# Optimization experiments

Measured on AMD Instinct MI355X. Metric: run time of the kernel, lower is better.

## Reference

```python
import jax, jax.numpy as jnp
import numpy as np
import math

T, B = 512, 32
QD, SD, H, NH = 128, 256, 512, 8
NQ, NS, NSUB = 30000, 400, 8
DKEY = QD + 2 * SD      # 640
DVAL = 4 * SD + QD      # 1152
P = H + 2 * SD + QD     # 1152 (pred_in_feature)
DH = H // NH            # 64
NEG = -1e32


def _layernorm(x, g, b, eps=1e-5):
    mu = jnp.mean(x, axis=-1, keepdims=True)
    var = jnp.mean((x - mu) ** 2, axis=-1, keepdims=True)
    return (x - mu) * jax.lax.rsqrt(var + eps) * g + b


def setup_inputs() -> dict:
    key = jax.random.key(0)
    ks = iter(jax.random.split(key, 48))
    def nrm(shape, scale=0.05):
        return (scale * jax.random.normal(next(ks), shape)).astype(jnp.float32)
    inp = {}
    inp['ans'] = jax.random.randint(next(ks), (T, B), 1, 5, dtype=jnp.int32)
    inp['correct_ans'] = jax.random.randint(next(ks), (T, B), 1, 5, dtype=jnp.int32)
    inp['labels'] = jax.random.randint(next(ks), (T, B), 0, 2, dtype=jnp.int32)
    inp['mask'] = jnp.ones((T, B), jnp.float32)
    inp['q_ids'] = jax.random.randint(next(ks), (T, B), 0, NQ, dtype=jnp.int32)
    inp['subject_ids'] = jax.random.randint(next(ks), (T, B, NSUB), 0, NS, dtype=jnp.int32)
    inp['subject_mask'] = (jax.random.uniform(next(ks), (T, B, NSUB)) < 0.7).astype(jnp.float32)
    inp['Eq'] = nrm((NQ, QD)); inp['Es'] = nrm((NS, SD))
    inp['Ea'] = nrm((4, SD)); inp['El'] = nrm((2, SD))
    inp['Wq'] = nrm((H, DKEY)); inp['bq'] = jnp.zeros((H,), jnp.float32)
    inp['Wk'] = nrm((H, DKEY)); inp['bk'] = jnp.zeros((H,), jnp.float32)
    inp['Wv'] = nrm((H, DVAL)); inp['bv'] = jnp.zeros((H,), jnp.float32)
    inp['Wo'] = nrm((H, H)); inp['bo'] = jnp.zeros((H,), jnp.float32)
    inp['ln1_g'] = jnp.ones((H,), jnp.float32); inp['ln1_b'] = jnp.zeros((H,), jnp.float32)
    inp['W1'] = nrm((H, H)); inp['b1'] = jnp.zeros((H,), jnp.float32)
    inp['W2'] = nrm((H, H)); inp['b2'] = jnp.zeros((H,), jnp.float32)
    inp['ln2_g'] = jnp.ones((H,), jnp.float32); inp['ln2_b'] = jnp.zeros((H,), jnp.float32)
    inp['gammas'] = jnp.zeros((NH, 1, 1), jnp.float32)
    inp['L1W'] = nrm((P, P)); inp['L1b'] = jnp.zeros((P,), jnp.float32)
    inp['L2W'] = nrm((P, P)); inp['L2b'] = jnp.zeros((P,), jnp.float32)
    inp['OW'] = nrm((1, P)); inp['Ob'] = jnp.zeros((1,), jnp.float32)
    return inp


def _forward(ans, correct_ans, labels, q_ids, subject_ids,
             mask, subject_mask, Eq, Es, Ea, El,
             Wq, bq, Wk, bk, Wv, bv, Wo, bo, ln1_g, ln1_b,
             W1, b1, W2, b2, ln2_g, ln2_b, gammas,
             L1W, L1b, L2W, L2b, OW, Ob):
    m3 = mask[:, :, None]                                   # [T,B,1]
    subjects = jnp.sum(Es[subject_ids] * subject_mask[..., None], axis=2)   # [T,B,SD]
    questions = Eq[q_ids]                                   # [T,B,QD]
    ans_embed = Ea[ans - 1] * m3
    ca_embed = Ea[correct_ans - 1]
    lab_embed = El[labels] * m3
    query = jnp.concatenate([questions, subjects, ca_embed], axis=-1)       # [T,B,DKEY]
    value = jnp.concatenate([lab_embed, ans_embed, ca_embed, questions, subjects], axis=-1)  # [T,B,DVAL]
    # note: original applies q_linear to kk and k_linear to qq (qq==kk==query here); akt=True => no pos-embed
    q = (query @ Wq.T + bq).reshape(T, B, NH, DH).transpose(1, 2, 0, 3)     # [B,NH,T,DH]
    k = (query @ Wk.T + bk).reshape(T, B, NH, DH).transpose(1, 2, 0, 3)
    v = (value @ Wv.T + bv).reshape(T, B, NH, DH).transpose(1, 2, 0, 3)
    scores = jnp.einsum('bhqd,bhkd->bhqk', q, k) / math.sqrt(DH)            # [B,NH,T,T]
    scores = jnp.where(mask.T[:, None, None, :] == 0, NEG, scores)
    # exponential distance decay (Softplus-gamma), applied AFTER the key-pad fill as in the original
    idx = jnp.arange(T)
    pe = jnp.sqrt(jnp.abs(idx[None, :] - idx[:, None]).astype(jnp.float32)) # [T,T]
    total_effect = jnp.clip(jnp.exp(pe[None] * (-jax.nn.softplus(gammas))), 1e-5, 1e5)  # [NH,T,T]
    scores = scores * total_effect[None]
    causal_bad = jnp.triu(jnp.ones((T, T), bool))            # upper incl. diagonal is masked
    scores = jnp.where(causal_bad, NEG, scores)
    scores = jax.nn.softmax(scores, axis=-1)
    scores = scores.at[:, :, 0, :].set(0.0)                  # pad-zero first query row
    attn = jnp.einsum('bhqk,bhkd->bhqd', scores, v)
    concat = attn.transpose(2, 0, 1, 3).reshape(T, B, H)
    out = _layernorm(concat @ Wo.T + bo, ln1_g, ln1_b)
    ffn = jax.nn.relu(out @ W1.T + b1) @ W2.T + b2
    out = out + _layernorm(ffn, ln2_g, ln2_b)
    pred = jnp.concatenate([out, questions, subjects, ca_embed], axis=-1)   # [T,B,P]
    h = jax.nn.relu(pred @ L1W.T + L1b)
    h = jax.nn.relu(h @ L2W.T + L2b)
    logits = ((h + pred) @ OW.T + Ob)[..., 0]                # [T,B]
    y = labels.astype(jnp.float32)
    bce = jnp.maximum(logits, 0.0) - logits * y + jnp.log1p(jnp.exp(-jnp.abs(logits)))
    loss = jnp.mean(bce * mask) / jnp.mean(mask)
    return loss


def reference(ans, correct_ans, labels, mask, q_ids, subject_ids, subject_mask,
              Eq, Es, Ea, El, Wq, bq, Wk, bk, Wv, bv, Wo, bo, ln1_g, ln1_b,
              W1, b1, W2, b2, ln2_g, ln2_b, gammas, L1W, L1b, L2W, L2b, OW, Ob):
    return _forward(ans, correct_ans, labels, q_ids, subject_ids,
                    mask, subject_mask, Eq, Es, Ea, El,
                    Wq, bq, Wk, bk, Wv, bv, Wo, bo, ln1_g, ln1_b,
                    W1, b1, W2, b2, ln2_g, ln2_b, gammas,
                    L1W, L1b, L2W, L2b, OW, Ob)
```

## Files before the change

kernel.cpp:

```cpp
#include <hip/hip_runtime.h>
#include <math.h>

#define T_LEN 512
#define B_SZ  32
#define NHEAD 8
#define DHEAD 64
#define H_DIM 512
#define TBTOK 16384
#define P_DIM 1152
#define P_PAD 1280

typedef unsigned short ushort_t;
typedef short short8 __attribute__((ext_vector_type(8)));
typedef float f32x4 __attribute__((ext_vector_type(4)));

__device__ __forceinline__ ushort_t f2bf(float f) {
    union { float f; unsigned int u; } v; v.f = f;
    unsigned int r = v.u + 0x7fffu + ((v.u >> 16) & 1u);
    return (ushort_t)(r >> 16);
}
__device__ __forceinline__ float bf2f(ushort_t h) {
    union { unsigned int u; float f; } v; v.u = ((unsigned int)h) << 16;
    return v.f;
}
__device__ __forceinline__ void gload_lds16(const void* g, void* l) {
    __builtin_amdgcn_global_load_lds(
        (const __attribute__((address_space(1))) void*)g,
        (__attribute__((address_space(3))) void*)l, 16, 0, 0);
}

__global__ __launch_bounds__(256) void convert_weights(
    const float* __restrict__ wq, const float* __restrict__ wk,
    const float* __restrict__ wv, const float* __restrict__ wo,
    const float* __restrict__ w1, const float* __restrict__ w2,
    ushort_t* __restrict__ dst, float* __restrict__ accum)
{
    if (blockIdx.x == 0 && threadIdx.x < 2) accum[threadIdx.x] = 0.f;
    const unsigned int offs[7] = {0u, 327680u, 655360u, 1245184u, 1507328u,
                                  1769472u, 2031616u};
    unsigned int c = (blockIdx.x * 256 + threadIdx.x) * 4;
    const float* srcs[6] = {wq, wk, wv, wo, w1, w2};
    int s = 0;
#pragma unroll
    for (int i = 0; i < 5; i++) s += (c >= offs[i + 1]) ? 1 : 0;
    float4 v = *(const float4*)(srcs[s] + (c - offs[s]));
    ushort4 o;
    o.x = f2bf(v.x); o.y = f2bf(v.y); o.z = f2bf(v.z); o.w = f2bf(v.w);
    *(ushort4*)(dst + c) = o;
}

__global__ __launch_bounds__(256) void pad_weights(
    const float* __restrict__ l1, const float* __restrict__ l2,
    const float* __restrict__ L1b, const float* __restrict__ L2b,
    const float* __restrict__ OW,
    ushort_t* __restrict__ l1d, ushort_t* __restrict__ l2d,
    float* __restrict__ L1bp, float* __restrict__ L2bp, float* __restrict__ OWp)
{
    int blk = blockIdx.x;
    if (blk < 1440) {
        int o4 = (blk * 256 + threadIdx.x) * 4;
        int row = o4 / 1152;
        int col = o4 - row * 1152;
        ushort4 o; o.x = 0; o.y = 0; o.z = 0; o.w = 0;
        if (row < 1152) {
            float4 v = *(const float4*)(l1 + (size_t)row * 1152 + col);
            o.x = f2bf(v.x); o.y = f2bf(v.y); o.z = f2bf(v.z); o.w = f2bf(v.w);
        }
        *(ushort4*)(l1d + o4) = o;
    } else if (blk < 3040) {
        int o4 = ((blk - 1440) * 256 + threadIdx.x) * 4;
        int row = o4 / 1280;
        int col = o4 - row * 1280;
        ushort4 o; o.x = 0; o.y = 0; o.z = 0; o.w = 0;
        if (row < 1152 && col < 1152) {
            float4 v = *(const float4*)(l2 + (size_t)row * 1152 + col);
            o.x = f2bf(v.x); o.y = f2bf(v.y); o.z = f2bf(v.z); o.w = f2bf(v.w);
        }
        *(ushort4*)(l2d + o4) = o;
    } else {
        for (int i = threadIdx.x; i < P_PAD; i += 256) {
            L1bp[i] = (i < P_DIM) ? L1b[i] : 0.f;
            L2bp[i] = (i < P_DIM) ? L2b[i] : 0.f;
            OWp[i]  = (i < P_DIM) ? OW[i]  : 0.f;
        }
    }
}

__global__ __launch_bounds__(256) void embed_kernel(
    const int* __restrict__ ans, const int* __restrict__ cans,
    const int* __restrict__ labels, const float* __restrict__ mask,
    const int* __restrict__ qids, const int* __restrict__ sids,
    const float* __restrict__ smask,
    const float* __restrict__ Eq, const float* __restrict__ Es,
    const float* __restrict__ Ea, const float* __restrict__ El,
    ushort_t* __restrict__ pred_bf, ushort_t* __restrict__ value_bf,
    const float* __restrict__ OW, const float* __restrict__ Ob,
    float* __restrict__ lgits)
{
    __shared__ float red[4];
    int m = blockIdx.x;
    int tid = threadIdx.x;
    float mval = mask[m];
    int qid = qids[m];
    int a   = ans[m] - 1;
    int ca  = cans[m] - 1;
    int lb  = labels[m];
    ushort_t* pr = pred_bf  + (size_t)m * P_DIM;
    ushort_t* vr = value_bf + (size_t)m * P_DIM;

    float part = 0.f;
    if (tid < 128) {
        ushort_t qv = f2bf(Eq[(size_t)qid * 128 + tid]);
        pr[512 + tid] = qv;
        vr[768 + tid] = qv;
        part = bf2f(qv) * OW[512 + tid];
    }
    int d = tid;
    float s = 0.f;
#pragma unroll
    for (int j = 0; j < 8; j++) {
        int  sid = sids[m * 8 + j];
        float sm = smask[m * 8 + j];
        s += Es[(size_t)sid * 256 + d] * sm;
    }
    ushort_t sb = f2bf(s);
    pr[640 + d] = sb;
    vr[896 + d] = sb;
    ushort_t cab = f2bf(Ea[ca * 256 + d]);
    pr[896 + d] = cab;
    vr[512 + d] = cab;
    vr[256 + d] = f2bf(Ea[a * 256 + d] * mval);
    vr[0   + d] = f2bf(El[lb * 256 + d] * mval);

    part = fmaf(bf2f(sb),  OW[640 + d], part);
    part = fmaf(bf2f(cab), OW[896 + d], part);
#pragma unroll
    for (int off = 32; off >= 1; off >>= 1) part += __shfl_xor(part, off, 64);
    if ((tid & 63) == 0) red[tid >> 6] = part;
    __syncthreads();
    if (tid == 0) lgits[m] = red[0] + red[1] + red[2] + red[3] + Ob[0];
}

template<int JC, int MODE, bool RELU>
__global__ __launch_bounds__(512, 2) void gemm4p(
    const ushort_t* __restrict__ A, int lda,
    const ushort_t* __restrict__ W, int ldw,
    const float* __restrict__ bias, const float* __restrict__ bias2,
    ushort_t* __restrict__ Cb, ushort_t* __restrict__ Cb2, int ldc, int K,
    const float* __restrict__ OW, float* __restrict__ lg)
{
    constexpr int BN = JC * 64;
    __shared__ __align__(16) ushort_t As2[2][2][256 * 32];
    __shared__ __align__(16) ushort_t Bs2[2][2][BN * 32];

    const int m0 = blockIdx.x * 256;
    const int n0 = blockIdx.y * BN;
    const int tid  = threadIdx.x;
    const int wave = tid >> 6;
    const int lane = tid & 63;
    const int wm = wave >> 2, wn = wave & 3;
    const int fr   = lane & 15;
    const int quad = lane >> 4;
    const int csw  = ((quad + ((fr >> 1) & 3)) & 3) * 8;

    const int slr = lane >> 2;
    const int sc  = (((lane & 3) - ((lane >> 3) & 3)) & 3) * 8;
    const ushort_t* Asrc;
    size_t aRS;
    if (MODE == 4) {
        Asrc = A + ((size_t)(((m0 & 511) + slr) << 5) + (m0 >> 9)) * lda + sc;
        aRS  = (size_t)32 * lda;
    } else {
        Asrc = A + (size_t)(m0 + slr) * lda + sc;
        aRS  = (size_t)lda;
    }
    const ushort_t* Wsrc = W + (size_t)(n0 + slr) * ldw + sc;
    const int NT = K >> 6;

    auto stA = [&](int t, int kh) {
#pragma unroll
        for (int n = 0; n < 2; n++) {
            int rl = (wave + 8 * n) << 4;
            gload_lds16(Asrc + (size_t)rl * aRS + (t * 64 + kh * 32),
                        &As2[t & 1][kh][rl * 32]);
        }
    };
    auto stB = [&](int t, int kh) {
#pragma unroll
        for (int n = 0; n < JC / 2; n++) {
            int rl = (wave + 8 * n) << 4;
            gload_lds16(Wsrc + (size_t)rl * ldw + (t * 64 + kh * 32),
                        &Bs2[t & 1][kh][rl * 32]);
        }
        if (JC & 1) {
            if (wave < 4) {
                int rl = (wave + 8 * (JC / 2)) << 4;
                gload_lds16(Wsrc + (size_t)rl * ldw + (t * 64 + kh * 32),
                            &Bs2[t & 1][kh][rl * 32]);
            }
        }
    };
    auto waitSteady = [&]() {
        if (JC == 2)      asm volatile("s_waitcnt vmcnt(3)" ::: "memory");
        else if (JC == 4) asm volatile("s_waitcnt vmcnt(4)" ::: "memory");
        else {
            if (wave < 4) asm volatile("s_waitcnt vmcnt(5)" ::: "memory");
            else          asm volatile("s_waitcnt vmcnt(4)" ::: "memory");
        }
    };

    f32x4 acc[8][JC] = {};

    stA(0, 0); stB(0, 0); stA(0, 1); stB(0, 1);
    if (NT > 1) { stA(1, 0); stB(1, 0); }
    if (NT > 2) waitSteady();
    else        asm volatile("s_waitcnt vmcnt(0)" ::: "memory");
    __builtin_amdgcn_s_barrier();

    short8 af[4], ag[4], bf[JC];
    for (int t = 0; t < NT; ++t) {
        const int db = t & 1;
        const ushort_t* Ar0 = &As2[db][0][0];
        const ushort_t* Ar1 = &As2[db][1][0];
        const ushort_t* Br0 = &Bs2[db][0][0];
        const ushort_t* Br1 = &Bs2[db][1][0];

#pragma unroll
        for (int i = 0; i < 4; i++)
            af[i] = *(const short8*)&Ar0[(wm * 128 + i * 16 + fr) * 32 + csw];
#pragma unroll
        for (int j = 0; j < JC; j++)
            bf[j] = *(const short8*)&Br0[(wn * (JC * 16) + j * 16 + fr) * 32 + csw];
        if (t + 1 < NT) stA(t + 1, 1);
#pragma unroll
        for (int i = 0; i < 4; i++)
#pragma unroll
            for (int j = 0; j < JC; j++)
                acc[i][j] = __builtin_amdgcn_mfma_f32_16x16x32_bf16(
                    af[i], bf[j], acc[i][j], 0, 0, 0);
#pragma unroll
        for (int i = 0; i < 4; i++)
            ag[i] = *(const short8*)&Ar0[(wm * 128 + 64 + i * 16 + fr) * 32 + csw];
        if (t + 1 < NT) stB(t + 1, 1);
#pragma unroll
        for (int i = 0; i < 4; i++)
#pragma unroll
            for (int j = 0; j < JC; j++)
                acc[4 + i][j] = __builtin_amdgcn_mfma_f32_16x16x32_bf16(
                    ag[i], bf[j], acc[4 + i][j], 0, 0, 0);
        __builtin_amdgcn_s_barrier();

#pragma unroll
        for (int i = 0; i < 4; i++)
            af[i] = *(const short8*)&Ar1[(wm * 128 + i * 16 + fr) * 32 + csw];
#pragma unroll
        for (int j = 0; j < JC; j++)
            bf[j] = *(const short8*)&Br1[(wn * (JC * 16) + j * 16 + fr) * 32 + csw];
        if (t + 2 < NT) stA(t + 2, 0);
#pragma unroll
        for (int i = 0; i < 4; i++)
#pragma unroll
            for (int j = 0; j < JC; j++)
                acc[i][j] = __builtin_amdgcn_mfma_f32_16x16x32_bf16(
                    af[i], bf[j], acc[i][j], 0, 0, 0);
#pragma unroll
        for (int i = 0; i < 4; i++)
            ag[i] = *(const short8*)&Ar1[(wm * 128 + 64 + i * 16 + fr) * 32 + csw];
        if (t + 2 < NT) stB(t + 2, 0);
#pragma unroll
        for (int i = 0; i < 4; i++)
#pragma unroll
            for (int j = 0; j < JC; j++)
                acc[4 + i][j] = __builtin_amdgcn_mfma_f32_16x16x32_bf16(
                    ag[i], bf[j], acc[4 + i][j], 0, 0, 0);
        if (t + 2 < NT) waitSteady();
        else            asm volatile("s_waitcnt vmcnt(0)" ::: "memory");
        __builtin_amdgcn_s_barrier();
    }

    const int nbase = n0 + wn * (JC * 16);

    if (MODE == 3) {
#pragma unroll
        for (int ii = 0; ii < 8; ii++)
#pragma unroll
            for (int r = 0; r < 4; r++) {
                int row = m0 + wm * 128 + (ii >> 2) * 64 + (ii & 3) * 16 + quad * 4 + r;
                float part = 0.f;
#pragma unroll
                for (int j = 0; j < JC; j++) {
                    int col = nbase + j * 16 + fr;
                    float v = fmaxf(acc[ii][j][r] + bias[col], 0.f);
                    part = fmaf(v, OW[col], part);
                }
                part += __shfl_xor(part, 1, 64);
                part += __shfl_xor(part, 2, 64);
                part += __shfl_xor(part, 4, 64);
                part += __shfl_xor(part, 8, 64);
                if (fr == 0) atomicAdd(&lg[row], part);
            }
        return;
    }

    if (MODE == 5) {
        bool side = (nbase >= 512);
        const float* bp = side ? bias2 : bias;
        const int boff  = nbase & 511;
        const float scl = side ? 1.f : 0.125f;
        ushort_t* base  = side ? Cb2 : Cb;
        const int h = (nbase >> 6) & 7;
        ushort_t* etw = ((ushort_t*)As2) + wave * (16 * 72);
#pragma unroll
        for (int ii = 0; ii < 8; ii++) {
#pragma unroll
            for (int r = 0; r < 4; r++)
#pragma unroll
                for (int j = 0; j < 4; j++) {
                    float v = (acc[ii][j][r] + bp[boff + j * 16 + fr]) * scl;
                    etw[(quad * 4 + r) * 72 + j * 16 + fr] = f2bf(v);
                }
            int rowb = m0 + wm * 128 + (ii >> 2) * 64 + (ii & 3) * 16;
#pragma unroll
            for (int u = lane; u < 128; u += 64) {
                int rr = u >> 3, cc = (u & 7) * 8;
                int row = rowb + rr;
                int tq = row >> 5, b = row & 31;
                short8 val = *(const short8*)&etw[rr * 72 + cc];
                *(short8*)&base[(((size_t)(b * 8 + h)) << 15) + ((size_t)tq << 6) + cc] = val;
            }
        }
        return;
    }

    if (MODE == 4) {
        ushort_t* etw = ((ushort_t*)As2) + wave * (32 * 72);
        const int h = nbase >> 6;
        const int dbase = nbase & 63;
#pragma unroll
        for (int mh = 0; mh < 2; mh++) {
#pragma unroll
            for (int i = 0; i < 4; i++)
#pragma unroll
                for (int r = 0; r < 4; r++) {
                    int rl = i * 16 + quad * 4 + r;
#pragma unroll
                    for (int j = 0; j < 2; j++) {
                        int cl = j * 16 + fr;
                        float v = acc[mh * 4 + i][j][r] + bias[nbase + cl];
                        etw[cl * 72 + rl] = f2bf(v);
                    }
                }
            int mbase = m0 + wm * 128 + mh * 64;
            int b = mbase >> 9, t0 = mbase & 511;
            size_t obase = (((size_t)(b * 8 + h)) << 15) + ((size_t)dbase << 9) + t0;
#pragma unroll
            for (int u = lane; u < 256; u += 64) {
                int dr = u >> 3, cc = (u & 7) * 8;
                short8 val = *(const short8*)&etw[dr * 72 + cc];
                *(short8*)&Cb[obase + ((size_t)dr << 9) + cc] = val;
            }
        }
        return;
    }

    {
        constexpr int STR = JC * 16 + 8;
        constexpr int CPR = 2 * JC;
        ushort_t* etw = ((ushort_t*)As2) + wave * (16 * STR);
#pragma unroll
        for (int ii = 0; ii < 8; ii++) {
#pragma unroll
            for (int r = 0; r < 4; r++)
#pragma unroll
                for (int j = 0; j < JC; j++) {
                    float v = acc[ii][j][r] + bias[nbase + j * 16 + fr];
                    if (RELU) v = fmaxf(v, 0.f);
                    etw[(quad * 4 + r) * STR + j * 16 + fr] = f2bf(v);
                }
            int rowb = m0 + wm * 128 + (ii >> 2) * 64 + (ii & 3) * 16;
#pragma unroll
            for (int u = lane; u < 16 * CPR; u += 64) {
                int rr = u / CPR;
                int cc = u - rr * CPR;
                short8 val = *(const short8*)&etw[rr * STR + cc * 8];
                *(short8*)&Cb[(size_t)(rowb + rr) * ldc + nbase + cc * 8] = val;
            }
        }
    }
}

__global__ __launch_bounds__(256) void attn_mfma(
    const ushort_t* __restrict__ qb, const ushort_t* __restrict__ kb,
    const ushort_t* __restrict__ vtb, const float* __restrict__ mask,
    const float* __restrict__ gammas, ushort_t* __restrict__ attnc)
{
    __shared__ __align__(16) ushort_t kbuf[2][64 * 64];
    __shared__ __align__(16) ushort_t vbuf[2][64 * 64];
    __shared__ __align__(16) ushort_t ps[4][16][72];
    __shared__ float decayF[512];
    __shared__ float mneg[512];

    const int bh  = blockIdx.x;
    const int b   = bh >> 3;
    const int h   = bh & 7;
    const int qt0 = (7 - blockIdx.y) * 64;
    const int tid  = threadIdx.x;
    const int wave = tid >> 6;
    const int lane = tid & 63;
    const int fr   = lane & 15;
    const int quad = lane >> 4;

    {
        float g  = gammas[h];
        float sp = (g > 20.f) ? g : log1pf(expf(g));
        for (int i = tid; i < 512; i += 256) {
            decayF[i] = fmaxf(exp2f(-sp * 1.44269504f * sqrtf((float)i)), 1e-5f)
                        * 1.44269504f;
            mneg[i]   = (mask[(size_t)i * B_SZ + b] == 0.f) ? -1e32f : 0.f;
        }
    }

    const int qr0 = qt0 + wave * 16;
    const ushort_t* qbase = qb  + ((size_t)bh << 15);
    const ushort_t* kbase = kb  + ((size_t)bh << 15);
    const ushort_t* vbase = vtb + ((size_t)bh << 15);

    short8 af0 = *(const short8*)(qbase + (size_t)(qr0 + fr) * 64 + quad * 8);
    short8 af1 = *(const short8*)(qbase + (size_t)(qr0 + fr) * 64 + 32 + quad * 8);
    const short8 ones = {0x3F80, 0x3F80, 0x3F80, 0x3F80,
                         0x3F80, 0x3F80, 0x3F80, 0x3F80};

    const int rl0 = wave * 16 + (lane >> 3);
    const int rl1 = rl0 + 8;
    const int sc0 = (((lane & 7) - rl0) & 7) * 8;
    const int sc1 = (((lane & 7) - rl1) & 7) * 8;

    auto stage = [&](int kt, int bufi) {
        gload_lds16(kbase + (size_t)(kt + rl0) * 64 + sc0, &kbuf[bufi][(wave * 16) * 64]);
        gload_lds16(kbase + (size_t)(kt + rl1) * 64 + sc1, &kbuf[bufi][(wave * 16 + 8) * 64]);
        gload_lds16(vbase + (size_t)rl0 * T_LEN + kt + sc0, &vbuf[bufi][(wave * 16) * 64]);
        gload_lds16(vbase + (size_t)rl1 * T_LEN + kt + sc1, &vbuf[bufi][(wave * 16 + 8) * 64]);
    };
    auto frag = [&](const ushort_t* buf, int row, int lchunk) -> short8 {
        return *(const short8*)&buf[row * 64 + ((lchunk + row) & 7) * 8];
    };

    stage(0, 0);

    f32x4 o[4] = {};
    f32x4 lacc = {};
    int bufi = 0;

    for (int kt0 = 0; kt0 <= qt0; kt0 += 64) {
        __syncthreads();
        if (kt0 < qt0) stage(kt0 + 64, bufi ^ 1);
        const bool diag = (kt0 == qt0);
        const ushort_t* kb_ = kbuf[bufi];
        const ushort_t* vb_ = vbuf[bufi];

        f32x4 sacc[4] = {};
#pragma unroll
        for (int j = 0; j < 4; j++) {
            int row = j * 16 + fr;
            short8 k0 = frag(kb_, row, quad);
            short8 k1 = frag(kb_, row, quad + 4);
            sacc[j] = __builtin_amdgcn_mfma_f32_16x16x32_bf16(af0, k0, sacc[j], 0, 0, 0);
            sacc[j] = __builtin_amdgcn_mfma_f32_16x16x32_bf16(af1, k1, sacc[j], 0, 0, 0);
        }

#pragma unroll
        for (int j = 0; j < 4; j++) {
            int kg = kt0 + j * 16 + fr;
            float mn = mneg[kg];
            int qgb = qr0 + quad * 4;
            if (!diag) {
                int base = qgb - kg;
#pragma unroll
                for (int r = 0; r < 4; r++) {
                    float t = fmaf(sacc[j][r], decayF[base + r], mn);
                    union { float f; unsigned u; } cv; cv.f = exp2f(t);
                    ps[wave][quad * 4 + r][j * 16 + fr] = (ushort_t)(cv.u >> 16);
                }
            } else {
#pragma unroll
                for (int r = 0; r < 4; r++) {
                    int didx = qgb + r - kg;
                    float dec = decayF[didx > 0 ? didx : 0];
                    float t = fmaf(sacc[j][r], dec, mn);
                    if (didx <= 0) t = -1e32f;
                    union { float f; unsigned u; } cv; cv.f = exp2f(t);
                    ps[wave][quad * 4 + r][j * 16 + fr] = (ushort_t)(cv.u >> 16);
                }
            }
        }
        short8 pf0 = *(const short8*)&ps[wave][fr][quad * 8];
        short8 pf1 = *(const short8*)&ps[wave][fr][32 + quad * 8];
        lacc = __builtin_amdgcn_mfma_f32_16x16x32_bf16(pf0, ones, lacc, 0, 0, 0);
        lacc = __builtin_amdgcn_mfma_f32_16x16x32_bf16(pf1, ones, lacc, 0, 0, 0);
#pragma unroll
        for (int j2 = 0; j2 < 4; j2++) {
            int row = j2 * 16 + fr;
            short8 v0 = frag(vb_, row, quad);
            short8 v1 = frag(vb_, row, quad + 4);
            o[j2] = __builtin_amdgcn_mfma_f32_16x16x32_bf16(pf0, v0, o[j2], 0, 0, 0);
            o[j2] = __builtin_amdgcn_mfma_f32_16x16x32_bf16(pf1, v1, o[j2], 0, 0, 0);
        }
        bufi ^= 1;
    }

#pragma unroll
    for (int r = 0; r < 4; r++) {
        int qg = qr0 + quad * 4 + r;
        float linv = (qg == 0) ? 0.f : 1.f / lacc[r];
#pragma unroll
        for (int j2 = 0; j2 < 4; j2++)
            ps[wave][quad * 4 + r][j2 * 16 + fr] = f2bf(o[j2][r] * linv);
    }
    const int sub8 = (lane & 7) * 8;
    const int grp  = lane >> 3;
#pragma unroll
    for (int half = 0; half < 2; half++) {
        int rowl = half * 8 + grp;
        short8 val = *(const short8*)&ps[wave][rowl][sub8];
        int qg = qr0 + rowl;
        *(short8*)&attnc[((size_t)qg * B_SZ + b) * H_DIM + h * DHEAD + sub8] = val;
    }
}

__global__ __launch_bounds__(256) void ln1_kernel(
    const ushort_t* __restrict__ X, const float* __restrict__ g,
    const float* __restrict__ bta, ushort_t* __restrict__ Yb)
{
    int m    = blockIdx.x * 4 + (threadIdx.x >> 6);
    int lane = threadIdx.x & 63;
    int c0   = lane * 8;
    const ushort_t* xr = X + (size_t)m * H_DIM + c0;
    float x[8];
    float s = 0.f, ss = 0.f;
    short8 xv = *(const short8*)xr;
#pragma unroll
    for (int i = 0; i < 8; i++) {
        x[i] = bf2f((ushort_t)xv[i]);
        s += x[i]; ss += x[i] * x[i];
    }
#pragma unroll
    for (int off = 32; off >= 1; off >>= 1) {
        s  += __shfl_xor(s,  off, 64);
        ss += __shfl_xor(ss, off, 64);
    }
    float mu  = s * (1.f / 512.f);
    float var = ss * (1.f / 512.f) - mu * mu;
    float rs  = rsqrtf(var + 1e-5f);
    ushort_t yb[8];
#pragma unroll
    for (int i = 0; i < 8; i++)
        yb[i] = f2bf((x[i] - mu) * rs * g[c0 + i] + bta[c0 + i]);
    *(short8*)(Yb + (size_t)m * H_DIM + c0) = *(short8*)&yb[0];
}

__global__ __launch_bounds__(256) void ln2_kernel(
    const ushort_t* __restrict__ X, const float* __restrict__ g,
    const float* __restrict__ bta, const ushort_t* __restrict__ res,
    ushort_t* __restrict__ pred_bf, const float* __restrict__ OW,
    float* __restrict__ lg)
{
    int m    = blockIdx.x * 4 + (threadIdx.x >> 6);
    int lane = threadIdx.x & 63;
    int c0   = lane * 8;
    const ushort_t* xr = X + (size_t)m * H_DIM + c0;
    float x[8];
    float s = 0.f, ss = 0.f;
    short8 xv = *(const short8*)xr;
#pragma unroll
    for (int i = 0; i < 8; i++) {
        x[i] = bf2f((ushort_t)xv[i]);
        s += x[i]; ss += x[i] * x[i];
    }
#pragma unroll
    for (int off = 32; off >= 1; off >>= 1) {
        s  += __shfl_xor(s,  off, 64);
        ss += __shfl_xor(ss, off, 64);
    }
    float mu  = s * (1.f / 512.f);
    float var = ss * (1.f / 512.f) - mu * mu;
    float rs  = rsqrtf(var + 1e-5f);
    short8 rv = *(const short8*)(res + (size_t)m * H_DIM + c0);
    ushort_t yb[8];
    float part = 0.f;
#pragma unroll
    for (int i = 0; i < 8; i++) {
        float v = (x[i] - mu) * rs * g[c0 + i] + bta[c0 + i] + bf2f((ushort_t)rv[i]);
        yb[i] = f2bf(v);
        part = fmaf(v, OW[c0 + i], part);
    }
    *(short8*)(pred_bf + (size_t)m * P_DIM + c0) = *(short8*)&yb[0];
#pragma unroll
    for (int off = 32; off >= 1; off >>= 1) part += __shfl_xor(part, off, 64);
    if (lane == 0) lg[m] += part;
}

__global__ __launch_bounds__(256) void bce_kernel(
    const float* __restrict__ lg, const int* __restrict__ labels,
    const float* __restrict__ mask, float* __restrict__ accum)
{
    int m    = blockIdx.x * 256 + threadIdx.x;
    int lane = threadIdx.x & 63;
    float l  = lg[m];
    float y  = (float)labels[m];
    float mv = mask[m];
    float a  = (fmaxf(l, 0.f) - l * y + log1pf(expf(-fabsf(l)))) * mv;
#pragma unroll
    for (int off = 32; off >= 1; off >>= 1) {
        a  += __shfl_xor(a,  off, 64);
        mv += __shfl_xor(mv, off, 64);
    }
    if (lane == 0) {
        atomicAdd(accum,     a);
        atomicAdd(accum + 1, mv);
    }
}

__global__ void finalize_kernel(const float* __restrict__ accum, float* __restrict__ out)
{
    out[0] = accum[0] / accum[1];
}

extern "C" void kernel_launch(void* const* d_in, const int* in_sizes, int n_in,
                              void* d_out, int out_size, void* d_ws, size_t ws_size,
                              hipStream_t stream)
{
    (void)in_sizes; (void)n_in; (void)out_size;
    const int*   ans    = (const int*)  d_in[0];
    const int*   cans   = (const int*)  d_in[1];
    const int*   labels = (const int*)  d_in[2];
    const float* mask   = (const float*)d_in[3];
    const int*   qids   = (const int*)  d_in[4];
    const int*   sids   = (const int*)  d_in[5];
    const float* smask  = (const float*)d_in[6];
    const float* Eq     = (const float*)d_in[7];
    const float* Es     = (const float*)d_in[8];
    const float* Ea     = (const float*)d_in[9];
    const float* El     = (const float*)d_in[10];
    const float* Wq     = (const float*)d_in[11];
    const float* bq     = (const float*)d_in[12];
    const float* Wk     = (const float*)d_in[13];
    const float* bk     = (const float*)d_in[14];
    const float* Wv     = (const float*)d_in[15];
    const float* bv     = (const float*)d_in[16];
    const float* Wo     = (const float*)d_in[17];
    const float* bo     = (const float*)d_in[18];
    const float* ln1_g  = (const float*)d_in[19];
    const float* ln1_b  = (const float*)d_in[20];
    const float* W1     = (const float*)d_in[21];
    const float* b1     = (const float*)d_in[22];
    const float* W2     = (const float*)d_in[23];
    const float* b2     = (const float*)d_in[24];
    const float* ln2_g  = (const float*)d_in[25];
    const float* ln2_b  = (const float*)d_in[26];
    const float* gammas = (const float*)d_in[27];
    const float* L1W    = (const float*)d_in[28];
    const float* L1b    = (const float*)d_in[29];
    const float* L2W    = (const float*)d_in[30];
    const float* L2b    = (const float*)d_in[31];
    const float* OW     = (const float*)d_in[32];
    const float* Ob     = (const float*)d_in[33];
    float* out = (float*)d_out;

    const size_t U = (size_t)TBTOK * 64;
    if (ws_size < 42 * U * sizeof(float)) return;
    float* ws = (float*)d_ws;
    ushort_t* wtb      = (ushort_t*)(ws);
    ushort_t* pred_bf  = (ushort_t*)(ws + 3 * U);
    ushort_t* value_bf = (ushort_t*)(ws + 12 * U);
    ushort_t* qb       = (ushort_t*)(ws + 21 * U);
    ushort_t* kb       = (ushort_t*)(ws + 25 * U);
    ushort_t* vtb      = (ushort_t*)(ws + 29 * U);
    ushort_t* attnc_bf = (ushort_t*)(ws + 33 * U);
    ushort_t* x1_bf    = (ushort_t*)(ws + 12 * U);
    ushort_t* out1_bf  = (ushort_t*)(ws + 24 * U);
    ushort_t* f1_bf    = (ushort_t*)(ws + 28 * U);
    ushort_t* f2_bf    = (ushort_t*)(ws + 32 * U);
    ushort_t* h1_bf    = (ushort_t*)(ws + 12 * U);
    float*    lgits    = ws + 41 * U;
    float*    accum    = lgits + TBTOK;
    float*    OWp      = accum + 2;
    float*    L1bp     = OWp + P_PAD;
    float*    L2bp     = L1bp + P_PAD;

    ushort_t* wqk_b = wtb + 0;
    ushort_t* wv_b  = wtb + 655360;
    ushort_t* wo_b  = wtb + 1245184;
    ushort_t* w1_b  = wtb + 1507328;
    ushort_t* w2_b  = wtb + 1769472;
    ushort_t* l1_b  = wtb + 2031616;
    ushort_t* l2_b  = wtb + 3506176;

    convert_weights<<<1984, 256, 0, stream>>>(Wq, Wk, Wv, Wo, W1, W2, wtb, accum);
    pad_weights<<<3041, 256, 0, stream>>>(L1W, L2W, L1b, L2b, OW,
                                          l1_b, l2_b, L1bp, L2bp, OWp);
    embed_kernel<<<TBTOK, 256, 0, stream>>>(ans, cans, labels, mask, qids, sids,
                                            smask, Eq, Es, Ea, El, pred_bf, value_bf,
                                            OW, Ob, lgits);
    gemm4p<4,5,false><<<dim3(64, 4), 512, 0, stream>>>(
        pred_bf + 512, P_DIM, wqk_b, 640, bq, bk, qb, kb, 0, 640, nullptr, nullptr);
    gemm4p<2,4,false><<<dim3(64, 4), 512, 0, stream>>>(
        value_bf, P_DIM, wv_b, P_DIM, bv, nullptr, vtb, nullptr, 0, P_DIM, nullptr, nullptr);
    attn_mfma<<<dim3(B_SZ * NHEAD, 8), 256, 0, stream>>>(
        qb, kb, vtb, mask, gammas, attnc_bf);
    gemm4p<2,1,false><<<dim3(64, 4), 512, 0, stream>>>(
        attnc_bf, H_DIM, wo_b, H_DIM, bo, nullptr, x1_bf, nullptr, H_DIM, H_DIM, nullptr, nullptr);
    ln1_kernel<<<TBTOK/4, 256, 0, stream>>>(x1_bf, ln1_g, ln1_b, out1_bf);
    gemm4p<2,1,true><<<dim3(64, 4), 512, 0, stream>>>(
        out1_bf, H_DIM, w1_b, H_DIM, b1, nullptr, f1_bf, nullptr, H_DIM, H_DIM, nullptr, nullptr);
    gemm4p<2,1,false><<<dim3(64, 4), 512, 0, stream>>>(
        f1_bf, H_DIM, w2_b, H_DIM, b2, nullptr, f2_bf, nullptr, H_DIM, H_DIM, nullptr, nullptr);
    ln2_kernel<<<TBTOK/4, 256, 0, stream>>>(f2_bf, ln2_g, ln2_b, out1_bf, pred_bf, OW, lgits);
    gemm4p<5,1,true><<<dim3(64, 4), 512, 0, stream>>>(
        pred_bf, P_DIM, l1_b, P_DIM, L1bp, nullptr, h1_bf, nullptr, P_PAD, P_DIM, nullptr, nullptr);
    gemm4p<5,3,true><<<dim3(64, 4), 512, 0, stream>>>(
        h1_bf, P_PAD, l2_b, P_PAD, L2bp, nullptr, nullptr, nullptr, 0, P_PAD, OWp, lgits);
    bce_kernel<<<TBTOK/256, 256, 0, stream>>>(lgits, labels, mask, accum);
    finalize_kernel<<<1, 1, 0, stream>>>(accum, out);
}
```

Before: 413.9 us.

## Shrink GEMM tile to 128 rows, single-buffer LDS and raise occupancy

Replaces the double-buffered 256-row GEMM with a 128-row tile that uses one LDS buffer, a full 64-wide K slab and a new 8-way swizzle. Launch bounds rise to 4 blocks per CU and grids double to 128x4, so the hardware overlaps loads across more resident blocks instead of relying on in-kernel prefetch. The cost is that each block now waits for its loads before computing, and each block reuses fewer rows of the weight tile.

Measured after the change: 405.7 us. 1.02x faster.

```diff
diff --git a/kernel.cpp b/kernel.cpp
--- a/kernel.cpp
+++ b/kernel.cpp
@@ -142,7 +142,7 @@
 }
 
 template<int JC, int MODE, bool RELU>
-__global__ __launch_bounds__(512, 2) void gemm4p(
+__global__ __launch_bounds__(512, 4) void gemmT(
     const ushort_t* __restrict__ A, int lda,
     const ushort_t* __restrict__ W, int ldw,
     const float* __restrict__ bias, const float* __restrict__ bias2,
@@ -150,25 +150,23 @@
     const float* __restrict__ OW, float* __restrict__ lg)
 {
     constexpr int BN = JC * 64;
-    __shared__ __align__(16) ushort_t As2[2][2][256 * 32];
-    __shared__ __align__(16) ushort_t Bs2[2][2][BN * 32];
-
-    const int m0 = blockIdx.x * 256;
+    __shared__ __align__(16) ushort_t SH[128 * 64 + BN * 64];
+    ushort_t* Bs = SH + 128 * 64;
+
+    const int m0 = blockIdx.x * 128;
     const int n0 = blockIdx.y * BN;
-    const int tid  = threadIdx.x;
-    const int wave = tid >> 6;
-    const int lane = tid & 63;
+    const int wave = threadIdx.x >> 6;
+    const int lane = threadIdx.x & 63;
     const int wm = wave >> 2, wn = wave & 3;
     const int fr   = lane & 15;
     const int quad = lane >> 4;
-    const int csw  = ((quad + ((fr >> 1) & 3)) & 3) * 8;
-
-    const int slr = lane >> 2;
-    const int sc  = (((lane & 3) - ((lane >> 3) & 3)) & 3) * 8;
+
+    const int slr = lane >> 3;
+    const int sc  = (((lane & 7) - ((wave * 4 + (slr >> 1)) & 7)) & 7) * 8;
     const ushort_t* Asrc;
     size_t aRS;
     if (MODE == 4) {
-        Asrc = A + ((size_t)(((m0 & 511) + slr) << 5) + (m0 >> 9)) * lda + sc;
+        Asrc = A + (size_t)(((m0 & 511) + slr) * 32 + (m0 >> 9)) * lda + sc;
         aRS  = (size_t)32 * lda;
     } else {
         Asrc = A + (size_t)(m0 + slr) * lda + sc;
@@ -177,115 +175,55 @@
     const ushort_t* Wsrc = W + (size_t)(n0 + slr) * ldw + sc;
     const int NT = K >> 6;
 
-    auto stA = [&](int t, int kh) {
+    auto stA = [&](int t) {
 #pragma unroll
         for (int n = 0; n < 2; n++) {
-            int rl = (wave + 8 * n) << 4;
-            gload_lds16(Asrc + (size_t)rl * aRS + (t * 64 + kh * 32),
-                        &As2[t & 1][kh][rl * 32]);
+            int rb = (wave + 8 * n) * 8;
+            gload_lds16(Asrc + (size_t)rb * aRS + t * 64, &SH[rb * 64]);
         }
     };
-    auto stB = [&](int t, int kh) {
-#pragma unroll
-        for (int n = 0; n < JC / 2; n++) {
-            int rl = (wave + 8 * n) << 4;
-            gload_lds16(Wsrc + (size_t)rl * ldw + (t * 64 + kh * 32),
-                        &Bs2[t & 1][kh][rl * 32]);
-        }
-        if (JC & 1) {
-            if (wave < 4) {
-                int rl = (wave + 8 * (JC / 2)) << 4;
-                gload_lds16(Wsrc + (size_t)rl * ldw + (t * 64 + kh * 32),
-                            &Bs2[t & 1][kh][rl * 32]);
-            }
+    auto stB = [&](int t) {
+#pragma unroll
+        for (int n = 0; n < JC; n++) {
+            int rb = (wave + 8 * n) * 8;
+            gload_lds16(Wsrc + (size_t)rb * ldw + t * 64, &Bs[rb * 64]);
         }
     };
-    auto waitSteady = [&]() {
-        if (JC == 2)      asm volatile("s_waitcnt vmcnt(3)" ::: "memory");
-        else if (JC == 4) asm volatile("s_waitcnt vmcnt(4)" ::: "memory");
-        else {
-            if (wave < 4) asm volatile("s_waitcnt vmcnt(5)" ::: "memory");
-            else          asm volatile("s_waitcnt vmcnt(4)" ::: "memory");
-        }
-    };
-
-    f32x4 acc[8][JC] = {};
-
-    stA(0, 0); stB(0, 0); stA(0, 1); stB(0, 1);
-    if (NT > 1) { stA(1, 0); stB(1, 0); }
-    if (NT > 2) waitSteady();
-    else        asm volatile("s_waitcnt vmcnt(0)" ::: "memory");
-    __builtin_amdgcn_s_barrier();
-
-    short8 af[4], ag[4], bf[JC];
+
+    f32x4 acc[4][JC] = {};
+
     for (int t = 0; t < NT; ++t) {
-        const int db = t & 1;
-        const ushort_t* Ar0 = &As2[db][0][0];
-        const ushort_t* Ar1 = &As2[db][1][0];
-        const ushort_t* Br0 = &Bs2[db][0][0];
-        const ushort_t* Br1 = &Bs2[db][1][0];
-
-#pragma unroll
-        for (int i = 0; i < 4; i++)
-            af[i] = *(const short8*)&Ar0[(wm * 128 + i * 16 + fr) * 32 + csw];
-#pragma unroll
-        for (int j = 0; j < JC; j++)
-            bf[j] = *(const short8*)&Br0[(wn * (JC * 16) + j * 16 + fr) * 32 + csw];
-        if (t + 1 < NT) stA(t + 1, 1);
-#pragma unroll
-        for (int i = 0; i < 4; i++)
+        stA(t); stB(t);
+        asm volatile("s_waitcnt vmcnt(0)" ::: "memory");
+        __builtin_amdgcn_s_barrier();
+#pragma unroll
+        for (int h = 0; h < 2; h++) {
+            const int cs = ((h * 4 + quad + (fr >> 1)) & 7) * 8;
+            short8 af[4], bf[JC];
+#pragma unroll
+            for (int i = 0; i < 4; i++)
+                af[i] = *(const short8*)&SH[(wm * 64 + i * 16 + fr) * 64 + cs];
 #pragma unroll
             for (int j = 0; j < JC; j++)
-                acc[i][j] = __builtin_amdgcn_mfma_f32_16x16x32_bf16(
-                    af[i], bf[j], acc[i][j], 0, 0, 0);
-#pragma unroll
-        for (int i = 0; i < 4; i++)
-            ag[i] = *(const short8*)&Ar0[(wm * 128 + 64 + i * 16 + fr) * 32 + csw];
-        if (t + 1 < NT) stB(t + 1, 1);
-#pragma unroll
-        for (int i = 0; i < 4; i++)
-#pragma unroll
-            for (int j = 0; j < JC; j++)
-                acc[4 + i][j] = __builtin_amdgcn_mfma_f32_16x16x32_bf16(
-                    ag[i], bf[j], acc[4 + i][j], 0, 0, 0);
+                bf[j] = *(const short8*)&Bs[(wn * (JC * 16) + j * 16 + fr) * 64 + cs];
+#pragma unroll
+            for (int i = 0; i < 4; i++)
+#pragma unroll
+                for (int j = 0; j < JC; j++)
+                    acc[i][j] = __builtin_amdgcn_mfma_f32_16x16x32_bf16(
+                        af[i], bf[j], acc[i][j], 0, 0, 0);
+        }
         __builtin_amdgcn_s_barrier();
-
-#pragma unroll
-        for (int i = 0; i < 4; i++)
-            af[i] = *(const short8*)&Ar1[(wm * 128 + i * 16 + fr) * 32 + csw];
-#pragma unroll
-        for (int j = 0; j < JC; j++)
-            bf[j] = *(const short8*)&Br1[(wn * (JC * 16) + j * 16 + fr) * 32 + csw];
-        if (t + 2 < NT) stA(t + 2, 0);
-#pragma unroll
-        for (int i = 0; i < 4; i++)
-#pragma unroll
-            for (int j = 0; j < JC; j++)
-                acc[i][j] = __builtin_amdgcn_mfma_f32_16x16x32_bf16(
-                    af[i], bf[j], acc[i][j], 0, 0, 0);
-#pragma unroll
-        for (int i = 0; i < 4; i++)
-            ag[i] = *(const short8*)&Ar1[(wm * 128 + 64 + i * 16 + fr) * 32 + csw];
-        if (t + 2 < NT) stB(t + 2, 0);
-#pragma unroll
-        for (int i = 0; i < 4; i++)
-#pragma unroll
-            for (int j = 0; j < JC; j++)
-                acc[4 + i][j] = __builtin_amdgcn_mfma_f32_16x16x32_bf16(
-                    ag[i], bf[j], acc[4 + i][j], 0, 0, 0);
-        if (t + 2 < NT) waitSteady();
-        else            asm volatile("s_waitcnt vmcnt(0)" ::: "memory");
-        __builtin_amdgcn_s_barrier();
     }
 
     const int nbase = n0 + wn * (JC * 16);
 
     if (MODE == 3) {
 #pragma unroll
-        for (int ii = 0; ii < 8; ii++)
+        for (int ii = 0; ii < 4; ii++)
 #pragma unroll
             for (int r = 0; r < 4; r++) {
-                int row = m0 + wm * 128 + (ii >> 2) * 64 + (ii & 3) * 16 + quad * 4 + r;
+                int row = m0 + wm * 64 + ii * 16 + quad * 4 + r;
                 float part = 0.f;
 #pragma unroll
                 for (int j = 0; j < JC; j++) {
@@ -309,9 +247,9 @@
         const float scl = side ? 1.f : 0.125f;
         ushort_t* base  = side ? Cb2 : Cb;
         const int h = (nbase >> 6) & 7;
-        ushort_t* etw = ((ushort_t*)As2) + wave * (16 * 72);
-#pragma unroll
-        for (int ii = 0; ii < 8; ii++) {
+        ushort_t* etw = SH + wave * (16 * 72);
+#pragma unroll
+        for (int ii = 0; ii < 4; ii++) {
 #pragma unroll
             for (int r = 0; r < 4; r++)
 #pragma unroll
@@ -319,7 +257,7 @@
                     float v = (acc[ii][j][r] + bp[boff + j * 16 + fr]) * scl;
                     etw[(quad * 4 + r) * 72 + j * 16 + fr] = f2bf(v);
                 }
-            int rowb = m0 + wm * 128 + (ii >> 2) * 64 + (ii & 3) * 16;
+            int rowb = m0 + wm * 64 + ii * 16;
 #pragma unroll
             for (int u = lane; u < 128; u += 64) {
                 int rr = u >> 3, cc = (u & 7) * 8;
@@ -333,30 +271,34 @@
     }
 
     if (MODE == 4) {
-        ushort_t* etw = ((ushort_t*)As2) + wave * (32 * 72);
+        ushort_t* etw = SH + wave * (32 * 40);
         const int h = nbase >> 6;
         const int dbase = nbase & 63;
-#pragma unroll
-        for (int mh = 0; mh < 2; mh++) {
-#pragma unroll
-            for (int i = 0; i < 4; i++)
+        const int mbase = m0 + wm * 64;
+        const int b = mbase >> 9;
+        size_t obase0 = (((size_t)(b * 8 + h)) << 15) + ((size_t)dbase << 9)
+                        + (mbase & 511);
+#pragma unroll
+        for (int p = 0; p < 2; p++) {
+#pragma unroll
+            for (int iiL = 0; iiL < 2; iiL++) {
+                int ii = p * 2 + iiL;
 #pragma unroll
                 for (int r = 0; r < 4; r++) {
-                    int rl = i * 16 + quad * 4 + r;
+                    int rl = iiL * 16 + quad * 4 + r;
 #pragma unroll
                     for (int j = 0; j < 2; j++) {
                         int cl = j * 16 + fr;
-                        float v = acc[mh * 4 + i][j][r] + bias[nbase + cl];
-                        etw[cl * 72 + rl] = f2bf(v);
+                        float v = acc[ii][j][r] + bias[nbase + cl];
+                        etw[cl * 40 + rl] = f2bf(v);
                     }
                 }
-            int mbase = m0 + wm * 128 + mh * 64;
-            int b = mbase >> 9, t0 = mbase & 511;
-            size_t obase = (((size_t)(b * 8 + h)) << 15) + ((size_t)dbase << 9) + t0;
-#pragma unroll
-            for (int u = lane; u < 256; u += 64) {
-                int dr = u >> 3, cc = (u & 7) * 8;
-                short8 val = *(const short8*)&etw[dr * 72 + cc];
+            }
+            size_t obase = obase0 + p * 32;
+#pragma unroll
+            for (int u = lane; u < 128; u += 64) {
+                int dr = u >> 2, cc = (u & 3) * 8;
+                short8 val = *(const short8*)&etw[dr * 40 + cc];
                 *(short8*)&Cb[obase + ((size_t)dr << 9) + cc] = val;
             }
         }
@@ -366,9 +308,9 @@
     {
         constexpr int STR = JC * 16 + 8;
         constexpr int CPR = 2 * JC;
-        ushort_t* etw = ((ushort_t*)As2) + wave * (16 * STR);
-#pragma unroll
-        for (int ii = 0; ii < 8; ii++) {
+        ushort_t* etw = SH + wave * (16 * STR);
+#pragma unroll
+        for (int ii = 0; ii < 4; ii++) {
 #pragma unroll
             for (int r = 0; r < 4; r++)
 #pragma unroll
@@ -377,7 +319,7 @@
                     if (RELU) v = fmaxf(v, 0.f);
                     etw[(quad * 4 + r) * STR + j * 16 + fr] = f2bf(v);
                 }
-            int rowb = m0 + wm * 128 + (ii >> 2) * 64 + (ii & 3) * 16;
+            int rowb = m0 + wm * 64 + ii * 16;
 #pragma unroll
             for (int u = lane; u < 16 * CPR; u += 64) {
                 int rr = u / CPR;
@@ -701,23 +643,23 @@
     embed_kernel<<<TBTOK, 256, 0, stream>>>(ans, cans, labels, mask, qids, sids,
                                             smask, Eq, Es, Ea, El, pred_bf, value_bf,
                                             OW, Ob, lgits);
-    gemm4p<4,5,false><<<dim3(64, 4), 512, 0, stream>>>(
+    gemmT<4,5,false><<<dim3(128, 4), 512, 0, stream>>>(
         pred_bf + 512, P_DIM, wqk_b, 640, bq, bk, qb, kb, 0, 640, nullptr, nullptr);
-    gemm4p<2,4,false><<<dim3(64, 4), 512, 0, stream>>>(
+    gemmT<2,4,false><<<dim3(128, 4), 512, 0, stream>>>(
         value_bf, P_DIM, wv_b, P_DIM, bv, nullptr, vtb, nullptr, 0, P_DIM, nullptr, nullptr);
     attn_mfma<<<dim3(B_SZ * NHEAD, 8), 256, 0, stream>>>(
         qb, kb, vtb, mask, gammas, attnc_bf);
-    gemm4p<2,1,false><<<dim3(64, 4), 512, 0, stream>>>(
+    gemmT<2,1,false><<<dim3(128, 4), 512, 0, stream>>>(
         attnc_bf, H_DIM, wo_b, H_DIM, bo, nullptr, x1_bf, nullptr, H_DIM, H_DIM, nullptr, nullptr);
     ln1_kernel<<<TBTOK/4, 256, 0, stream>>>(x1_bf, ln1_g, ln1_b, out1_bf);
-    gemm4p<2,1,true><<<dim3(64, 4), 512, 0, stream>>>(
+    gemmT<2,1,true><<<dim3(128, 4), 512, 0, stream>>>(
         out1_bf, H_DIM, w1_b, H_DIM, b1, nullptr, f1_bf, nullptr, H_DIM, H_DIM, nullptr, nullptr);
-    gemm4p<2,1,false><<<dim3(64, 4), 512, 0, stream>>>(
+    gemmT<2,1,false><<<dim3(128, 4), 512, 0, stream>>>(
         f1_bf, H_DIM, w2_b, H_DIM, b2, nullptr, f2_bf, nullptr, H_DIM, H_DIM, nullptr, nullptr);
     ln2_kernel<<<TBTOK/4, 256, 0, stream>>>(f2_bf, ln2_g, ln2_b, out1_bf, pred_bf, OW, lgits);
-    gemm4p<5,1,true><<<dim3(64, 4), 512, 0, stream>>>(
+    gemmT<5,1,true><<<dim3(128, 4), 512, 0, stream>>>(
         pred_bf, P_DIM, l1_b, P_DIM, L1bp, nullptr, h1_bf, nullptr, P_PAD, P_DIM, nullptr, nullptr);
-    gemm4p<5,3,true><<<dim3(64, 4), 512, 0, stream>>>(
+    gemmT<5,3,true><<<dim3(128, 4), 512, 0, stream>>>(
         h1_bf, P_PAD, l2_b, P_PAD, L2bp, nullptr, nullptr, nullptr, 0, P_PAD, OWp, lgits);
     bce_kernel<<<TBTOK/256, 256, 0, stream>>>(lgits, labels, mask, accum);
     finalize_kernel<<<1, 1, 0, stream>>>(accum, out);
```
